# Performance work log

Measured on AMD Instinct MI355X. Metric: run time of the kernel, lower is better.

## Reference

```python
import jax, jax.numpy as jnp
import numpy as np

N = 50000      # node_num
DIN = 128      # input_dim
DH = 128       # hidden_dim
DE = 128       # embedding_dim
DD = 128       # decoder_dim
NE = 800000    # num edges (before self loops)
B = 4096       # drug pairs
EPS = 1e-5


def setup_inputs() -> dict:
    key = jax.random.key(0)
    ks = jax.random.split(key, 16)
    x = jax.random.normal(ks[0], (N, DIN), jnp.float32)
    edge_index = jax.random.randint(ks[1], (2, NE), 0, N, dtype=jnp.int32)
    drug_index = jax.random.randint(ks[2], (B, 2), 0, N, dtype=jnp.int32)
    s = 0.05  # weight scale for numerical sanity
    return {
        "x": x,
        "edge_index": edge_index,
        "drug_index": drug_index,
        "w1": jax.random.normal(ks[3], (DIN, DH), jnp.float32) * s,
        "b1": jnp.zeros((DH,), jnp.float32),
        "w2": jax.random.normal(ks[4], (DH, DH), jnp.float32) * s,
        "b2": jnp.zeros((DH,), jnp.float32),
        "w3": jax.random.normal(ks[5], (DH, DE), jnp.float32) * s,
        "b3": jnp.zeros((DE,), jnp.float32),
        "g1": jnp.ones((DH,), jnp.float32), "be1": jnp.zeros((DH,), jnp.float32),
        "g2": jnp.ones((DH,), jnp.float32), "be2": jnp.zeros((DH,), jnp.float32),
        "g3": jnp.ones((DE,), jnp.float32), "be3": jnp.zeros((DE,), jnp.float32),
        "p1": jax.random.normal(ks[6], (DE, DD), jnp.float32) * s,
        "p2": jax.random.normal(ks[7], (DD, DD), jnp.float32) * s,
    }


def gcn_conv(x, row, col, W, b):
    # row/col already include self loops; PyG: message from row (source), aggregated at col (target)
    n = x.shape[0]
    h = x @ W + b                                   # linear first, as in GCNConv.forward
    deg = jnp.zeros((n,), h.dtype).at[col].add(1.0)  # degree(col) incl. self loops -> >= 1
    dis = deg ** -0.5
    norm = dis[row] * dis[col]                      # [E+N]
    msg = norm[:, None] * h[row]                    # [E+N, d] gather
    return jax.ops.segment_sum(msg, col, num_segments=n)  # scatter-add


def batch_norm(x, gamma, beta):
    m = jnp.mean(x, axis=0)
    v = jnp.mean((x - m) ** 2, axis=0)  # biased var, as torch BatchNorm training
    return (x - m) * jax.lax.rsqrt(v + EPS) * gamma + beta


def leaky(x):
    return jnp.where(x >= 0, x, 0.1 * x)  # LeakyReLU(0.1)


def reference(x, edge_index, drug_index, w1, b1, w2, b2, w3, b3,
              g1, be1, g2, be2, g3, be3, p1, p2):
    n = x.shape[0]
    self_loop = jnp.arange(n, dtype=edge_index.dtype)
    row = jnp.concatenate([edge_index[0], self_loop])
    col = jnp.concatenate([edge_index[1], self_loop])

    h = leaky(batch_norm(gcn_conv(x, row, col, w1, b1), g1, be1))
    h = leaky(batch_norm(gcn_conv(h, row, col, w2, b2), g2, be2))
    h = leaky(batch_norm(gcn_conv(h, row, col, w3, b3), g3, be3))

    di = drug_index.reshape(-1, 2)
    a = h[di[:, 0] - 1]  # [B, DE] (1-based indices; -1 wraps like torch negative index)
    bb = h[di[:, 1] - 1]  # [B, DE]
    t = a @ p1 @ p2 @ p1.T            # [B, DE] bilinear decode, batched
    ypred = jnp.sum(t * bb, axis=1, keepdims=True)  # [B, 1]
    return ypred
```

## Files before the change

### kernel.cpp

```cpp
#include <hip/hip_runtime.h>

#define PAD 64
#define NSLOT 64

__global__ void init_kernel(int* __restrict__ cnt, float* __restrict__ stats, int n, int nstat) {
  int i = blockIdx.x * blockDim.x + threadIdx.x;
  int stride = gridDim.x * blockDim.x;
  for (int j = i; j < n; j += stride) cnt[j] = 0;
  for (int j = i; j < nstat; j += stride) stats[j] = 0.f;
}

__global__ void fillcsr_kernel(const int* __restrict__ row, const int* __restrict__ col,
                               int* __restrict__ cnt, int* __restrict__ csr, int ne) {
  int e = blockIdx.x * blockDim.x + threadIdx.x;
  if (e < ne) {
    int d = col[e];
    int p = atomicAdd(&cnt[d], 1);
    if (p < PAD) csr[d * PAD + p] = row[e];
  }
}

__global__ __launch_bounds__(256, 4) void gemm_kernel(
    const float* __restrict__ A, const float* __restrict__ W, const float* __restrict__ bias,
    float* __restrict__ out, int n, float invN,
    const float* __restrict__ bn_sum, const float* __restrict__ bn_sq,
    const float* __restrict__ bn_g, const float* __restrict__ bn_b, int use_bn,
    const int* __restrict__ cnt) {
  __shared__ float Ws[32 * 128];
  __shared__ float xs[32 * 128];
  __shared__ float bnsc[128], bnsh[128];
  int tid = threadIdx.x;
  if (tid < 128) {
    if (use_bn) {
      float s = 0.f, q = 0.f;
      for (int r2 = 0; r2 < NSLOT; ++r2) { s += bn_sum[r2 * 128 + tid]; q += bn_sq[r2 * 128 + tid]; }
      float m = s * invN;
      float var = q * invN - m * m;
      float rs = rsqrtf(var + 1e-5f);
      float sc = rs * bn_g[tid];
      bnsc[tid] = sc;
      bnsh[tid] = bn_b[tid] - m * sc;
    } else {
      bnsc[tid] = 1.f; bnsh[tid] = 0.f;
    }
  }
  int base = blockIdx.x * 128;
  int tx = tid & 15, ty = tid >> 4;
  int c0 = tx * 4, r0 = ty * 4;
  int r = tid & 127;
  int row_s = base + r;
  int hf = tid >> 7;
  int kw = tid >> 5;
  int c4 = tid & 31;
  const float4* Arow = (const float4*)(A + (size_t)row_s * 128);
  float acc[8][8];
#pragma unroll
  for (int i = 0; i < 8; ++i)
#pragma unroll
    for (int j = 0; j < 8; ++j) acc[i][j] = 0.f;

  for (int kp = 0; kp < 4; ++kp) {
    __syncthreads();
#pragma unroll
    for (int it = 0; it < 4; ++it) {
      int kl = kw + it * 8;
      float4 wv = ((const float4*)(W + (size_t)(kp * 32 + kl) * 128))[c4];
      *(float4*)&Ws[kl * 128 + c4 * 4] = wv;
    }
#pragma unroll
    for (int it = 0; it < 4; ++it) {
      int kbl = hf + it * 2;
      float4 v = make_float4(0.f, 0.f, 0.f, 0.f);
      if (row_s < n) v = Arow[kp * 8 + kbl];
      if (use_bn) {
        int k0 = kp * 32 + kbl * 4;
        float t;
        t = v.x * bnsc[k0 + 0] + bnsh[k0 + 0]; v.x = t >= 0.f ? t : 0.1f * t;
        t = v.y * bnsc[k0 + 1] + bnsh[k0 + 1]; v.y = t >= 0.f ? t : 0.1f * t;
        t = v.z * bnsc[k0 + 2] + bnsh[k0 + 2]; v.z = t >= 0.f ? t : 0.1f * t;
        t = v.w * bnsc[k0 + 3] + bnsh[k0 + 3]; v.w = t >= 0.f ? t : 0.1f * t;
      }
      int kl = kbl * 4;
      xs[(kl + 0) * 128 + r] = v.x;
      xs[(kl + 1) * 128 + r] = v.y;
      xs[(kl + 2) * 128 + r] = v.z;
      xs[(kl + 3) * 128 + r] = v.w;
    }
    __syncthreads();
#pragma unroll 4
    for (int k = 0; k < 32; ++k) {
      float4 a0 = *(const float4*)&xs[k * 128 + r0];
      float4 a1 = *(const float4*)&xs[k * 128 + 64 + r0];
      float4 w0 = *(const float4*)&Ws[k * 128 + c0];
      float4 w1 = *(const float4*)&Ws[k * 128 + 64 + c0];
      float xr[8], wc[8];
      xr[0] = a0.x; xr[1] = a0.y; xr[2] = a0.z; xr[3] = a0.w;
      xr[4] = a1.x; xr[5] = a1.y; xr[6] = a1.z; xr[7] = a1.w;
      wc[0] = w0.x; wc[1] = w0.y; wc[2] = w0.z; wc[3] = w0.w;
      wc[4] = w1.x; wc[5] = w1.y; wc[6] = w1.z; wc[7] = w1.w;
#pragma unroll
      for (int i = 0; i < 8; ++i)
#pragma unroll
        for (int j = 0; j < 8; ++j)
          acc[i][j] = fmaf(xr[i], wc[j], acc[i][j]);
    }
  }
  float bb0[4], bb1[4];
#pragma unroll
  for (int j = 0; j < 4; ++j) { bb0[j] = bias[c0 + j]; bb1[j] = bias[64 + c0 + j]; }
#pragma unroll
  for (int i = 0; i < 8; ++i) {
    int row = base + (i < 4 ? r0 + i : 64 + r0 + (i - 4));
    if (row < n) {
      float rs = rsqrtf((float)(cnt[row] + 1));
      float4 o0, o1;
      o0.x = (acc[i][0] + bb0[0]) * rs; o0.y = (acc[i][1] + bb0[1]) * rs;
      o0.z = (acc[i][2] + bb0[2]) * rs; o0.w = (acc[i][3] + bb0[3]) * rs;
      o1.x = (acc[i][4] + bb1[0]) * rs; o1.y = (acc[i][5] + bb1[1]) * rs;
      o1.z = (acc[i][6] + bb1[2]) * rs; o1.w = (acc[i][7] + bb1[3]) * rs;
      *(float4*)&out[(size_t)row * 128 + c0] = o0;
      *(float4*)&out[(size_t)row * 128 + 64 + c0] = o1;
    }
  }
}

__global__ __launch_bounds__(256) void agg_kernel(const float* __restrict__ z,
                                                  const int* __restrict__ cnt,
                                                  const int* __restrict__ csr,
                                                  float* __restrict__ out,
                                                  float* __restrict__ Ssum,
                                                  float* __restrict__ Ssq,
                                                  int n, int half) {
  __shared__ float bs[4][128], bq[4][128];
  int tid = threadIdx.x;
  int lane = tid & 63;
  int wv = tid >> 6;
  int w = (blockIdx.x * blockDim.x + tid) >> 6;
  float stx = 0.f, sty = 0.f, qtx = 0.f, qty = 0.f;
  if (w < half) {
    int i0 = w, i1 = w + half;
    bool has1 = (i1 < n);
    const float2* __restrict__ h2 = (const float2*)z;
    unsigned off0 = (unsigned)i0 * 64u + (unsigned)lane;
    unsigned off1 = (unsigned)i1 * 64u + (unsigned)lane;
    float2 self0 = h2[off0];
    float2 self1 = has1 ? h2[off1] : make_float2(0.f, 0.f);
    int c0r = cnt[i0];
    int c1r = has1 ? cnt[i1] : 0;
    float d0 = rsqrtf((float)(c0r + 1));
    float d1 = rsqrtf((float)(c1r + 1));
    int e0 = c0r > PAD ? PAD : c0r;
    int e1 = c1r > PAD ? PAD : c1r;
    const int* __restrict__ lp0 = csr + (size_t)i0 * PAD;
    const int* __restrict__ lp1 = csr + (size_t)i1 * PAD;
    float s0x = self0.x, s0y = self0.y;
    float s1x = self1.x, s1y = self1.y;
    int my0 = (lane < e0) ? lp0[lane] : 0;
    int my1 = (lane < e1) ? lp1[lane] : 0;
    int p0 = 0, p1 = 0;
    while (p0 + 8 <= e0 && p1 + 8 <= e1) {
      float2 v0[8], v1[8];
#pragma unroll
      for (int u = 0; u < 8; ++u) { int s = __shfl(my0, p0 + u, 64); v0[u] = h2[(unsigned)s * 64u + (unsigned)lane]; }
#pragma unroll
      for (int u = 0; u < 8; ++u) { int s = __shfl(my1, p1 + u, 64); v1[u] = h2[(unsigned)s * 64u + (unsigned)lane]; }
#pragma unroll
      for (int u = 0; u < 8; ++u) {
        s0x += v0[u].x; s0y += v0[u].y;
        s1x += v1[u].x; s1y += v1[u].y;
      }
      p0 += 8; p1 += 8;
    }
    for (; p0 + 8 <= e0; p0 += 8) {
      float2 v[8];
#pragma unroll
      for (int u = 0; u < 8; ++u) { int s = __shfl(my0, p0 + u, 64); v[u] = h2[(unsigned)s * 64u + (unsigned)lane]; }
#pragma unroll
      for (int u = 0; u < 8; ++u) { s0x += v[u].x; s0y += v[u].y; }
    }
    for (; p0 + 4 <= e0; p0 += 4) {
      float2 v[4];
#pragma unroll
      for (int u = 0; u < 4; ++u) { int s = __shfl(my0, p0 + u, 64); v[u] = h2[(unsigned)s * 64u + (unsigned)lane]; }
#pragma unroll
      for (int u = 0; u < 4; ++u) { s0x += v[u].x; s0y += v[u].y; }
    }
    for (; p0 < e0; ++p0) {
      int s = __shfl(my0, p0, 64);
      float2 v = h2[(unsigned)s * 64u + (unsigned)lane];
      s0x += v.x; s0y += v.y;
    }
    for (; p1 + 8 <= e1; p1 += 8) {
      float2 v[8];
#pragma unroll
      for (int u = 0; u < 8; ++u) { int s = __shfl(my1, p1 + u, 64); v[u] = h2[(unsigned)s * 64u + (unsigned)lane]; }
#pragma unroll
      for (int u = 0; u < 8; ++u) { s1x += v[u].x; s1y += v[u].y; }
    }
    for (; p1 + 4 <= e1; p1 += 4) {
      float2 v[4];
#pragma unroll
      for (int u = 0; u < 4; ++u) { int s = __shfl(my1, p1 + u, 64); v[u] = h2[(unsigned)s * 64u + (unsigned)lane]; }
#pragma unroll
      for (int u = 0; u < 4; ++u) { s1x += v[u].x; s1y += v[u].y; }
    }
    for (; p1 < e1; ++p1) {
      int s = __shfl(my1, p1, 64);
      float2 v = h2[(unsigned)s * 64u + (unsigned)lane];
      s1x += v.x; s1y += v.y;
    }
    float2 o0; o0.x = d0 * s0x; o0.y = d0 * s0y;
    ((float2*)out)[off0] = o0;
    stx += o0.x; qtx = fmaf(o0.x, o0.x, qtx);
    sty += o0.y; qty = fmaf(o0.y, o0.y, qty);
    if (has1) {
      float2 o1; o1.x = d1 * s1x; o1.y = d1 * s1y;
      ((float2*)out)[off1] = o1;
      stx += o1.x; qtx = fmaf(o1.x, o1.x, qtx);
      sty += o1.y; qty = fmaf(o1.y, o1.y, qty);
    }
  }
  bs[wv][2 * lane] = stx;     bs[wv][2 * lane + 1] = sty;
  bq[wv][2 * lane] = qtx;     bq[wv][2 * lane + 1] = qty;
  __syncthreads();
  if (tid < 128) {
    float s = bs[0][tid] + bs[1][tid] + bs[2][tid] + bs[3][tid];
    float q = bq[0][tid] + bq[1][tid] + bq[2][tid] + bq[3][tid];
    int slot = (blockIdx.x & (NSLOT - 1)) * 128 + tid;
    atomicAdd(&Ssum[slot], s);
    atomicAdd(&Ssq[slot], q);
  }
}

__global__ __launch_bounds__(128) void mm128_kernel(const float* __restrict__ A, const float* __restrict__ B,
                                                    float* __restrict__ C, int transB) {
  __shared__ float Ar[128];
  int i = blockIdx.x, j = threadIdx.x;
  Ar[j] = A[i * 128 + j];
  __syncthreads();
  float acc = 0.f;
  if (transB) {
    for (int k = 0; k < 128; ++k) acc = fmaf(Ar[k], B[j * 128 + k], acc);
  } else {
    for (int k = 0; k < 128; ++k) acc = fmaf(Ar[k], B[k * 128 + j], acc);
  }
  C[i * 128 + j] = acc;
}

__global__ __launch_bounds__(256) void decoder_kernel(
    const float* __restrict__ h, const int* __restrict__ di, const float* __restrict__ M,
    const float* __restrict__ bn_sum, const float* __restrict__ bn_sq,
    const float* __restrict__ bn_g, const float* __restrict__ bn_b,
    float* __restrict__ out, int npairs, int n, float invN) {
  __shared__ float Ms[128 * 128];
  __shared__ float sc[128], sh[128];
  int tid = threadIdx.x;
  if (tid < 128) {
    float s = 0.f, q = 0.f;
    for (int r2 = 0; r2 < NSLOT; ++r2) { s += bn_sum[r2 * 128 + tid]; q += bn_sq[r2 * 128 + tid]; }
    float m = s * invN;
    float var = q * invN - m * m;
    float rs = rsqrtf(var + 1e-5f);
    float scv = rs * bn_g[tid];
    sc[tid] = scv;
    sh[tid] = bn_b[tid] - m * scv;
  }
  for (int t = tid; t < 4096; t += 256) ((float4*)Ms)[t] = ((const float4*)M)[t];
  __syncthreads();
  int lane = tid & 63, wv = tid >> 6;
  int wid = blockIdx.x * 4 + wv;
  int nw = gridDim.x * 4;
  for (int k = wid; k < npairs; k += nw) {
    int ia = di[2 * k] - 1;     if (ia < 0) ia += n;
    int ib = di[2 * k + 1] - 1; if (ib < 0) ib += n;
    const float* ap = h + (size_t)ia * 128;
    const float* bp = h + (size_t)ib * 128;
    float u0 = 0.f, u1 = 0.f;
#pragma unroll 8
    for (int i = 0; i < 128; ++i) {
      float av = ap[i] * sc[i] + sh[i];
      av = av >= 0.f ? av : 0.1f * av;
      u0 = fmaf(av, Ms[i * 128 + lane], u0);
      u1 = fmaf(av, Ms[i * 128 + 64 + lane], u1);
    }
    float b0 = bp[lane] * sc[lane] + sh[lane];            b0 = b0 >= 0.f ? b0 : 0.1f * b0;
    float b1 = bp[lane + 64] * sc[lane + 64] + sh[lane + 64]; b1 = b1 >= 0.f ? b1 : 0.1f * b1;
    float part = u0 * b0 + u1 * b1;
#pragma unroll
    for (int o = 32; o; o >>= 1) part += __shfl_down(part, o, 64);
    if (lane == 0) out[k] = part;
  }
}

extern "C" void kernel_launch(void* const* d_in, const int* in_sizes, int n_in,
                              void* d_out, int out_size, void* d_ws, size_t ws_size,
                              hipStream_t stream) {
  const float* x   = (const float*)d_in[0];
  const int*   ei  = (const int*)d_in[1];
  const int*   dri = (const int*)d_in[2];
  const float* w1  = (const float*)d_in[3];
  const float* b1  = (const float*)d_in[4];
  const float* w2  = (const float*)d_in[5];
  const float* b2  = (const float*)d_in[6];
  const float* w3  = (const float*)d_in[7];
  const float* b3  = (const float*)d_in[8];
  const float* g1  = (const float*)d_in[9];
  const float* be1 = (const float*)d_in[10];
  const float* g2  = (const float*)d_in[11];
  const float* be2 = (const float*)d_in[12];
  const float* g3  = (const float*)d_in[13];
  const float* be3 = (const float*)d_in[14];
  const float* p1  = (const float*)d_in[15];
  const float* p2  = (const float*)d_in[16];
  float* out = (float*)d_out;

  int n  = in_sizes[0] / 128;
  int ne = in_sizes[1] / 2;
  int np = in_sizes[2] / 2;
  const int* erow = ei;
  const int* ecol = ei + ne;

  size_t o = 0;
  char* wsb = (char*)d_ws;
  auto alloc = [&](size_t bytes) { void* p = wsb + o; o += (bytes + 255) & ~255ull; return p; };
  float* T1   = (float*)alloc((size_t)n * 128 * 4);
  float* T2   = (float*)alloc((size_t)n * 128 * 4);
  int*   csr  = (int*)alloc((size_t)n * PAD * 4);
  int*   cnt  = (int*)alloc((size_t)n * 4);
  int nstat = 6 * NSLOT * 128;
  float* stats = (float*)alloc((size_t)nstat * 4);
  float* M1   = (float*)alloc(128 * 128 * 4);
  float* M2   = (float*)alloc(128 * 128 * 4);
  float* Ssum1 = stats;
  float* Ssq1  = stats + 1 * NSLOT * 128;
  float* Ssum2 = stats + 2 * NSLOT * 128;
  float* Ssq2  = stats + 3 * NSLOT * 128;
  float* Ssum3 = stats + 4 * NSLOT * 128;
  float* Ssq3  = stats + 5 * NSLOT * 128;

  float invN = 1.0f / (float)n;
  int eb = (ne + 255) / 256;
  int gb = (n + 127) / 128;
  int half = (n + 1) / 2;
  int ab = (half + 3) / 4;

  init_kernel<<<512, 256, 0, stream>>>(cnt, stats, n, nstat);
  fillcsr_kernel<<<eb, 256, 0, stream>>>(erow, ecol, cnt, csr, ne);

  gemm_kernel<<<gb, 256, 0, stream>>>(x, w1, b1, T1, n, invN, nullptr, nullptr, nullptr, nullptr, 0, cnt);
  agg_kernel<<<ab, 256, 0, stream>>>(T1, cnt, csr, T2, Ssum1, Ssq1, n, half);

  gemm_kernel<<<gb, 256, 0, stream>>>(T2, w2, b2, T1, n, invN, Ssum1, Ssq1, g1, be1, 1, cnt);
  agg_kernel<<<ab, 256, 0, stream>>>(T1, cnt, csr, T2, Ssum2, Ssq2, n, half);

  gemm_kernel<<<gb, 256, 0, stream>>>(T2, w3, b3, T1, n, invN, Ssum2, Ssq2, g2, be2, 1, cnt);
  agg_kernel<<<ab, 256, 0, stream>>>(T1, cnt, csr, T2, Ssum3, Ssq3, n, half);

  mm128_kernel<<<128, 128, 0, stream>>>(p1, p2, M1, 0);
  mm128_kernel<<<128, 128, 0, stream>>>(M1, p1, M2, 1);
  decoder_kernel<<<256, 256, 0, stream>>>(T2, dri, M2, Ssum3, Ssq3, g3, be3, out, np, n, invN);
}
```

Before: 383.4 us.

## Fuse bilinear matrix kernels, move stats zeroing, shuffle-broadcast decoder inputs

Folds the two mm128 launches into one kernel that stages p2 and then p1 in padded shared memory to build M2 = p1·p2·p1ᵀ in a single pass. Zeroing of the BN stats buffers moves from init_kernel into fillcsr_kernel. The decoder now loads each 'a' row as one coalesced float2 per lane and broadcasts it with wave shuffles, instead of having every lane redundantly read the whole row from global memory. The goal is fewer launches and less redundant memory traffic on small tail kernels, at the cost of extra shuffle instructions in the decoder.

```diff
diff --git a/kernel.cpp b/kernel.cpp
--- a/kernel.cpp
+++ b/kernel.cpp
@@ -3,20 +3,22 @@
 #define PAD 64
 #define NSLOT 64
 
-__global__ void init_kernel(int* __restrict__ cnt, float* __restrict__ stats, int n, int nstat) {
+__global__ void init_kernel(int* __restrict__ cnt, int n) {
   int i = blockIdx.x * blockDim.x + threadIdx.x;
   int stride = gridDim.x * blockDim.x;
   for (int j = i; j < n; j += stride) cnt[j] = 0;
-  for (int j = i; j < nstat; j += stride) stats[j] = 0.f;
 }
 
 __global__ void fillcsr_kernel(const int* __restrict__ row, const int* __restrict__ col,
-                               int* __restrict__ cnt, int* __restrict__ csr, int ne) {
-  int e = blockIdx.x * blockDim.x + threadIdx.x;
-  if (e < ne) {
-    int d = col[e];
+                               int* __restrict__ cnt, int* __restrict__ csr, int ne,
+                               float* __restrict__ stats, int nstat) {
+  int gid = blockIdx.x * blockDim.x + threadIdx.x;
+  int stride = gridDim.x * blockDim.x;
+  for (int j = gid; j < nstat; j += stride) stats[j] = 0.f;
+  if (gid < ne) {
+    int d = col[gid];
     int p = atomicAdd(&cnt[d], 1);
-    if (p < PAD) csr[d * PAD + p] = row[e];
+    if (p < PAD) csr[d * PAD + p] = row[gid];
   }
 }
 
@@ -232,19 +234,43 @@
   }
 }
 
-__global__ __launch_bounds__(128) void mm128_kernel(const float* __restrict__ A, const float* __restrict__ B,
-                                                    float* __restrict__ C, int transB) {
-  __shared__ float Ar[128];
-  int i = blockIdx.x, j = threadIdx.x;
-  Ar[j] = A[i * 128 + j];
-  __syncthreads();
-  float acc = 0.f;
-  if (transB) {
-    for (int k = 0; k < 128; ++k) acc = fmaf(Ar[k], B[j * 128 + k], acc);
-  } else {
-    for (int k = 0; k < 128; ++k) acc = fmaf(Ar[k], B[k * 128 + j], acc);
-  }
-  C[i * 128 + j] = acc;
+__global__ __launch_bounds__(128) void bilinear_m_kernel(const float* __restrict__ p1,
+                                                         const float* __restrict__ p2,
+                                                         float* __restrict__ M2) {
+  __shared__ float Bs[128 * 129];
+  __shared__ float rr[128];
+  __shared__ float tmp[128];
+  int i = blockIdx.x, t = threadIdx.x;
+  rr[t] = p1[i * 128 + t];
+  const float4* p24 = (const float4*)p2;
+#pragma unroll 8
+  for (int it = 0; it < 32; ++it) {
+    int f4 = t + 128 * it;
+    int k = f4 >> 5, c = f4 & 31;
+    float4 v = p24[f4];
+    float* d = &Bs[k * 129 + c * 4];
+    d[0] = v.x; d[1] = v.y; d[2] = v.z; d[3] = v.w;
+  }
+  __syncthreads();
+  float a0 = 0.f;
+#pragma unroll 8
+  for (int k = 0; k < 128; ++k) a0 = fmaf(rr[k], Bs[k * 129 + t], a0);
+  __syncthreads();
+  tmp[t] = a0;
+  const float4* p14 = (const float4*)p1;
+#pragma unroll 8
+  for (int it = 0; it < 32; ++it) {
+    int f4 = t + 128 * it;
+    int k = f4 >> 5, c = f4 & 31;
+    float4 v = p14[f4];
+    float* d = &Bs[k * 129 + c * 4];
+    d[0] = v.x; d[1] = v.y; d[2] = v.z; d[3] = v.w;
+  }
+  __syncthreads();
+  float a1 = 0.f;
+#pragma unroll 8
+  for (int l = 0; l < 128; ++l) a1 = fmaf(tmp[l], Bs[t * 129 + l], a1);
+  M2[i * 128 + t] = a1;
 }
 
 __global__ __launch_bounds__(256) void decoder_kernel(
@@ -273,17 +299,23 @@
   for (int k = wid; k < npairs; k += nw) {
     int ia = di[2 * k] - 1;     if (ia < 0) ia += n;
     int ib = di[2 * k + 1] - 1; if (ib < 0) ib += n;
-    const float* ap = h + (size_t)ia * 128;
+    const float2* ap2 = (const float2*)(h + (size_t)ia * 128);
     const float* bp = h + (size_t)ib * 128;
+    float2 a2 = ap2[lane];
+    float ax = a2.x * sc[2 * lane] + sh[2 * lane];         ax = ax >= 0.f ? ax : 0.1f * ax;
+    float ay = a2.y * sc[2 * lane + 1] + sh[2 * lane + 1]; ay = ay >= 0.f ? ay : 0.1f * ay;
     float u0 = 0.f, u1 = 0.f;
 #pragma unroll 8
-    for (int i = 0; i < 128; ++i) {
-      float av = ap[i] * sc[i] + sh[i];
-      av = av >= 0.f ? av : 0.1f * av;
-      u0 = fmaf(av, Ms[i * 128 + lane], u0);
-      u1 = fmaf(av, Ms[i * 128 + 64 + lane], u1);
-    }
-    float b0 = bp[lane] * sc[lane] + sh[lane];            b0 = b0 >= 0.f ? b0 : 0.1f * b0;
+    for (int i2 = 0; i2 < 64; ++i2) {
+      float avx = __shfl(ax, i2, 64);
+      float avy = __shfl(ay, i2, 64);
+      int i = 2 * i2;
+      u0 = fmaf(avx, Ms[i * 128 + lane], u0);
+      u1 = fmaf(avx, Ms[i * 128 + 64 + lane], u1);
+      u0 = fmaf(avy, Ms[(i + 1) * 128 + lane], u0);
+      u1 = fmaf(avy, Ms[(i + 1) * 128 + 64 + lane], u1);
+    }
+    float b0 = bp[lane] * sc[lane] + sh[lane];                b0 = b0 >= 0.f ? b0 : 0.1f * b0;
     float b1 = bp[lane + 64] * sc[lane + 64] + sh[lane + 64]; b1 = b1 >= 0.f ? b1 : 0.1f * b1;
     float part = u0 * b0 + u1 * b1;
 #pragma unroll
@@ -329,7 +361,6 @@
   int*   cnt  = (int*)alloc((size_t)n * 4);
   int nstat = 6 * NSLOT * 128;
   float* stats = (float*)alloc((size_t)nstat * 4);
-  float* M1   = (float*)alloc(128 * 128 * 4);
   float* M2   = (float*)alloc(128 * 128 * 4);
   float* Ssum1 = stats;
   float* Ssq1  = stats + 1 * NSLOT * 128;
@@ -344,8 +375,8 @@
   int half = (n + 1) / 2;
   int ab = (half + 3) / 4;
 
-  init_kernel<<<512, 256, 0, stream>>>(cnt, stats, n, nstat);
-  fillcsr_kernel<<<eb, 256, 0, stream>>>(erow, ecol, cnt, csr, ne);
+  init_kernel<<<256, 256, 0, stream>>>(cnt, n);
+  fillcsr_kernel<<<eb, 256, 0, stream>>>(erow, ecol, cnt, csr, ne, stats, nstat);
 
   gemm_kernel<<<gb, 256, 0, stream>>>(x, w1, b1, T1, n, invN, nullptr, nullptr, nullptr, nullptr, 0, cnt);
   agg_kernel<<<ab, 256, 0, stream>>>(T1, cnt, csr, T2, Ssum1, Ssq1, n, half);
@@ -356,7 +387,6 @@
   gemm_kernel<<<gb, 256, 0, stream>>>(T2, w3, b3, T1, n, invN, Ssum2, Ssq2, g2, be2, 1, cnt);
   agg_kernel<<<ab, 256, 0, stream>>>(T1, cnt, csr, T2, Ssum3, Ssq3, n, half);
 
-  mm128_kernel<<<128, 128, 0, stream>>>(p1, p2, M1, 0);
-  mm128_kernel<<<128, 128, 0, stream>>>(M1, p1, M2, 1);
+  bilinear_m_kernel<<<128, 128, 0, stream>>>(p1, p2, M2);
   decoder_kernel<<<256, 256, 0, stream>>>(T2, dri, M2, Ssum3, Ssq3, g3, be3, out, np, n, invN);
 }
```

Measured after the change: 373.1 us. -2.7%, faster.
